# Kernel optimization log

Hardware: AMD Instinct MI355X
Metric: run time of the kernel (lower is better)

Reference implementation:

```python
import jax, jax.numpy as jnp
import numpy as np

EMB = 1024
HEADS = 16
EPS = 1e-6


def setup_inputs() -> dict:
    key = jax.random.key(0)
    ks = jax.random.split(key, 11)
    B, T = 4, 2048
    s = 0.02
    inp = {
        "x": jax.random.normal(ks[0], (B, T, EMB), dtype=jnp.float32),
        "Wq": jax.random.normal(ks[1], (EMB, EMB), dtype=jnp.float32) * s,
        "bq": jnp.zeros((EMB,), dtype=jnp.float32),
        "Wk": jax.random.normal(ks[2], (EMB, EMB), dtype=jnp.float32) * s,
        "bk": jnp.zeros((EMB,), dtype=jnp.float32),
        "Wv": jax.random.normal(ks[3], (EMB, EMB), dtype=jnp.float32) * s,
        "bv": jnp.zeros((EMB,), dtype=jnp.float32),
        "Wp": jax.random.normal(ks[4], (EMB, EMB), dtype=jnp.float32) * s,
        "bp": jnp.zeros((EMB,), dtype=jnp.float32),
        "gamma": jnp.ones((EMB,), dtype=jnp.float32),
        "beta": jnp.zeros((EMB,), dtype=jnp.float32),
    }
    return inp


def reference(x, Wq, bq, Wk, bk, Wv, bv, Wp, bp, gamma, beta):
    B, T, E = x.shape
    H = HEADS
    hd = E // H
    residual = x
    # torch Linear: y = x @ W.T + b
    q = (jnp.einsum('bte,fe->btf', x, Wq) + bq).reshape(B, T, H, hd).transpose(0, 2, 1, 3)
    k = (jnp.einsum('bte,fe->btf', x, Wk) + bk).reshape(B, T, H, hd).transpose(0, 2, 1, 3)
    v = (jnp.einsum('bte,fe->btf', x, Wv) + bv).reshape(B, T, H, hd).transpose(0, 2, 1, 3)
    # NOTE: original scales by 1/sqrt(T), not 1/sqrt(head_size)
    scale = 1.0 / jnp.sqrt(jnp.asarray(T, dtype=x.dtype))
    att = jnp.einsum('bhqd,bhkd->bhqk', q, k) * scale
    causal = jnp.tril(jnp.ones((T, T), dtype=bool))
    att = jnp.where(causal, att, -jnp.inf)
    att = jax.nn.softmax(att, axis=-1)
    out = jnp.einsum('bhqk,bhkd->bhqd', att, v)
    out = out.transpose(0, 2, 1, 3).reshape(B, T, E)
    # residual added BEFORE projection (as in original)
    out = jnp.einsum('bte,fe->btf', out + residual, Wp) + bp
    # LayerNorm(eps=1e-6)
    mu = jnp.mean(out, axis=-1, keepdims=True)
    var = jnp.mean(jnp.square(out - mu), axis=-1, keepdims=True)
    out = (out - mu) / jnp.sqrt(var + EPS) * gamma + beta
    return out
```

## Files before the change

### kernel.cpp

```cpp
#include <hip/hip_runtime.h>
#include <hip/hip_bf16.h>
#include <cstdint>
#include <cstdio>

#define EMB    1024
#define HEADS  16
#define HD     64
#define TSEQ   2048
#define NBATCH 4
#define BT     (NBATCH*TSEQ)
#define QKVN   3072
#define QKLD   2048

#define CSCALE (1.4426950408889634f * 0.022097086912079608f)

typedef __hip_bfloat16 bf16;
typedef __attribute__((ext_vector_type(8))) short short8;
typedef __attribute__((ext_vector_type(4))) short short4v;
typedef __attribute__((ext_vector_type(4))) float f32x4;

#define MFMA32(A,B,C) __builtin_amdgcn_mfma_f32_16x16x32_bf16(A,B,C,0,0,0)
#if __has_builtin(__builtin_amdgcn_mfma_f32_16x16x16_bf16)
#define MFMA16(A,B,C) __builtin_amdgcn_mfma_f32_16x16x16_bf16(A,B,C,0,0,0)
#else
#define MFMA16(A,B,C) __builtin_amdgcn_mfma_f32_16x16x16bf16_1k(A,B,C,0,0,0)
#endif

#if __has_builtin(__builtin_amdgcn_exp2f)
#define EXP2(x) __builtin_amdgcn_exp2f(x)
#else
#define EXP2(x) exp2f(x)
#endif

template<bool B> struct BoolC { static constexpr bool value = B; };

__device__ __forceinline__ void gload_lds16(const void* g, void* l) {
  __builtin_amdgcn_global_load_lds(
      (const __attribute__((address_space(1))) void*)g,
      (__attribute__((address_space(3))) void*)l,
      16, 0, 0);
}

__device__ __forceinline__ unsigned pkbf(float a, float b) {
  unsigned ua = __builtin_bit_cast(unsigned, a) + 0x8000u;
  unsigned ub = __builtin_bit_cast(unsigned, b) + 0x8000u;
  return __builtin_amdgcn_perm(ub, ua, 0x07060302u);
}

#define BARRIER() do { asm volatile("" ::: "memory"); \
                       __builtin_amdgcn_s_barrier(); \
                       asm volatile("" ::: "memory"); } while (0)
#define BAR_VM(N) do { asm volatile("s_waitcnt vmcnt(" #N ")" ::: "memory"); \
                       __builtin_amdgcn_s_barrier(); \
                       asm volatile("" ::: "memory"); } while (0)

__global__ void fused_cast(const float* __restrict__ x, const float* __restrict__ Wq,
                           const float* __restrict__ Wk, const float* __restrict__ Wv,
                           const float* __restrict__ Wp, const float* __restrict__ bq,
                           const float* __restrict__ bk, const float* __restrict__ bv,
                           bf16* __restrict__ xb, bf16* __restrict__ wqkv,
                           bf16* __restrict__ wpb, float* __restrict__ biasqkv) {
  const int blk = blockIdx.x;
  const int i = threadIdx.x * 4;
  if (blk >= 12288) {
    const int wsel = blk - 12288;
    const float* bsrc = wsel == 0 ? bq : (wsel == 1 ? bk : bv);
    float4 bv4 = *(const float4*)(bsrc + i);
    if (wsel == 0) { bv4.x *= CSCALE; bv4.y *= CSCALE; bv4.z *= CSCALE; bv4.w *= CSCALE; }
    *(float4*)(biasqkv + wsel * 1024 + i) = bv4;
    return;
  }
  const float* src; bf16* dst; float sc = 1.0f;
  if (blk < 8192)       { src = x  + (size_t)blk * 1024;           dst = xb   + (size_t)blk * 1024; }
  else if (blk < 9216)  { src = Wq + (size_t)(blk - 8192) * 1024;  dst = wqkv + (size_t)(blk - 8192) * 1024; sc = CSCALE; }
  else if (blk < 10240) { src = Wk + (size_t)(blk - 9216) * 1024;  dst = wqkv + ((size_t)1 << 20) + (size_t)(blk - 9216) * 1024; }
  else if (blk < 11264) { src = Wv + (size_t)(blk - 10240) * 1024; dst = wqkv + ((size_t)2 << 20) + (size_t)(blk - 10240) * 1024; }
  else                  { src = Wp + (size_t)(blk - 11264) * 1024; dst = wpb  + (size_t)(blk - 11264) * 1024; }
  float4 v = *(const float4*)(src + i);
  union { short4v v; bf16 b[4]; } u;
  u.b[0] = __float2bfloat16(v.x * sc); u.b[1] = __float2bfloat16(v.y * sc);
  u.b[2] = __float2bfloat16(v.z * sc); u.b[3] = __float2bfloat16(v.w * sc);
  *(short4v*)(dst + i) = u.v;
}

#define PHASE_MFMA(MI0, NJ0) do { \
  __builtin_amdgcn_s_setprio(1); \
  _Pragma("unroll") \
  for (int m2 = 0; m2 < 4; ++m2) { \
    _Pragma("unroll") \
    for (int n2 = 0; n2 < 2; ++n2) { \
      acc[(MI0)+m2][(NJ0)+n2] = MFMA32(af[m2][0], bfr[(NJ0)+n2][0], acc[(MI0)+m2][(NJ0)+n2]); \
      acc[(MI0)+m2][(NJ0)+n2] = MFMA32(af[m2][1], bfr[(NJ0)+n2][1], acc[(MI0)+m2][(NJ0)+n2]); \
    } \
  } \
  __builtin_amdgcn_s_setprio(0); \
} while (0)

#define TILE(T, P) { \
  const int kn = ((T) + 1) * 64; \
  const bool st = (T) < 15; \
  const char* aB = rdA + (P) * 32768; \
  const char* bB = rdB + (P) * 32768; \
  char* sA = ldsA + ((P) ^ 1) * 32768 + wbase; \
  char* sB = ldsB + ((P) ^ 1) * 32768 + wbase; \
   \
  _Pragma("unroll") \
  for (int m2 = 0; m2 < 4; ++m2) { \
    af[m2][0] = *(const short8*)(aB + m2 * 2048 + cs0); \
    af[m2][1] = *(const short8*)(aB + m2 * 2048 + cs1); \
  } \
  _Pragma("unroll") \
  for (int n2 = 0; n2 < 2; ++n2) { \
    bfr[n2][0] = *(const short8*)(bB + n2 * 2048 + cs0); \
    bfr[n2][1] = *(const short8*)(bB + n2 * 2048 + cs1); \
  } \
  if (st) { gload_lds16(gB + kn,          sB);         \
            gload_lds16(gB + 131072 + kn, sB + 16384); } \
  BARRIER(); \
  PHASE_MFMA(0, 0); \
  BARRIER(); \
   \
  _Pragma("unroll") \
  for (int n2 = 2; n2 < 4; ++n2) { \
    bfr[n2][0] = *(const short8*)(bB + n2 * 2048 + cs0); \
    bfr[n2][1] = *(const short8*)(bB + n2 * 2048 + cs1); \
  } \
  if (st) { gload_lds16(gA + kn,          sA);         \
            gload_lds16(gA + 131072 + kn, sA + 16384); } \
  BARRIER(); \
  PHASE_MFMA(0, 2); \
  if (st) { BAR_VM(4); } else { BAR_VM(0); } \
   \
  _Pragma("unroll") \
  for (int m2 = 0; m2 < 4; ++m2) { \
    af[m2][0] = *(const short8*)(aB + (4 + m2) * 2048 + cs0); \
    af[m2][1] = *(const short8*)(aB + (4 + m2) * 2048 + cs1); \
  } \
  if (st) { gload_lds16(gB + 65536 + kn,  sB + 8192);  \
            gload_lds16(gB + 196608 + kn, sB + 24576); } \
  BARRIER(); \
  PHASE_MFMA(4, 2); \
  BARRIER(); \
   \
  if (st) { gload_lds16(gA + 65536 + kn,  sA + 8192);  \
            gload_lds16(gA + 196608 + kn, sA + 24576); } \
  PHASE_MFMA(4, 0); \
  if (st) { BAR_VM(2); } \
}

__global__ __launch_bounds__(512, 2) void gemm_qkv8(
    const bf16* __restrict__ A, const bf16* __restrict__ B,
    const float* __restrict__ bias, bf16* __restrict__ qkout,
    bf16* __restrict__ vt) {
  __shared__ short smem[65536];
  const int tid = threadIdx.x;
  const int l = tid & 63, w = tid >> 6;
  const int r = l & 15, qd = l >> 4;
  const int wm = w >> 2, wn = w & 3;

  const int f0 = blockIdx.x;
  const int sid = (f0 & 7) * 48 + (f0 >> 3);
  const int m0 = (sid / 12) * 256;
  const int n0 = (sid % 12) * 256;

  const int rowA = tid >> 3;
  const int chk = (tid & 7) ^ (rowA & 7);
  const bf16* gA = A + (size_t)(m0 + rowA) * 1024 + chk * 8;
  const bf16* gB = B + (size_t)(n0 + rowA) * 1024 + chk * 8;
  char* ldsA = (char*)smem;
  char* ldsB = (char*)smem + 65536;
  const int wbase = w * 1024;

  const char* rdA = (const char*)smem + wm * 16384 + r * 128;
  const char* rdB = (const char*)smem + 65536 + (wn >> 1) * 16384 +
                    ((wn & 1) * 64 + r) * 128;
  const int cs0 = (qd ^ (r & 7)) * 16;
  const int cs1 = ((4 + qd) ^ (r & 7)) * 16;

  f32x4 acc[8][4];
#pragma unroll
  for (int i = 0; i < 8; ++i)
#pragma unroll
    for (int j = 0; j < 4; ++j) acc[i][j] = (f32x4){0.f, 0.f, 0.f, 0.f};
  short8 af[4][2], bfr[4][2];

  {
    char* sA = ldsA + wbase;
    char* sB = ldsB + wbase;
    gload_lds16(gB,          sB);
    gload_lds16(gB + 131072, sB + 16384);
    gload_lds16(gA,          sA);
    gload_lds16(gA + 131072, sA + 16384);
    gload_lds16(gB + 65536,  sB + 8192);
    gload_lds16(gB + 196608, sB + 24576);
    gload_lds16(gA + 65536,  sA + 8192);
    gload_lds16(gA + 196608, sA + 24576);
    BAR_VM(2);
  }

#pragma unroll 1
  for (int tt = 0; tt < 8; ++tt) {
    TILE(tt * 2, 0)
    TILE(tt * 2 + 1, 1)
  }

  if (n0 < 2048) {
#pragma unroll
    for (int nt = 0; nt < 4; ++nt) {
      const int col = n0 + wn * 64 + nt * 16 + r;
      const float bv = bias[col];
#pragma unroll
      for (int mi = 0; mi < 8; ++mi) {
#pragma unroll
        for (int reg = 0; reg < 4; ++reg) {
          const int row = m0 + wm * 128 + mi * 16 + qd * 4 + reg;
          qkout[(size_t)row * QKLD + col] = __float2bfloat16(acc[mi][nt][reg] + bv);
        }
      }
    }
  } else {
    char* img = (char*)smem;
#pragma unroll
    for (int nt = 0; nt < 4; ++nt) {
      const int c_local = wn * 64 + nt * 16 + r;
      const float bv = bias[n0 + c_local];
      const int d7 = c_local & 7;
#pragma unroll
      for (int mi = 0; mi < 8; ++mi) {
        const int tbase = wm * 128 + mi * 16 + qd * 4;
        const int chunk = tbase >> 6;
        const int sbits = ((tbase >> 3) ^ d7) & 7;
        union { short4v v; bf16 b[4]; } u;
#pragma unroll
        for (int reg = 0; reg < 4; ++reg)
          u.b[reg] = __float2bfloat16(acc[mi][nt][reg] + bv);
        *(short4v*)(img + c_local * 512 + chunk * 128 + sbits * 16 + (qd & 1) * 8) = u.v;
      }
    }
    __syncthreads();
    const int bb = m0 >> 11, tb = m0 & 2047;
    const int hb = (n0 - 2048) >> 6;
    const int off = (tid & 31) * 16;
#pragma unroll
    for (int i = 0; i < 16; ++i) {
      const int row = i * 16 + (tid >> 5);
      const int h2 = hb + (row >> 6), d = row & 63;
      const f32x4 vv = *(const f32x4*)(img + row * 512 + off);
      char* dst = (char*)(vt + ((size_t)(bb * 16 + h2) * 64 + d) * 2048 + tb) + off;
      *(f32x4*)dst = vv;
    }
  }
}

#define PJ_MFMA(MI0) do { \
  __builtin_amdgcn_s_setprio(1); \
  _Pragma("unroll") \
  for (int m2 = 0; m2 < 2; ++m2) { \
    _Pragma("unroll") \
    for (int nj = 0; nj < 2; ++nj) { \
      acc[(MI0)+m2][nj] = MFMA32(af[m2][0], bfr[nj][0], acc[(MI0)+m2][nj]); \
      acc[(MI0)+m2][nj] = MFMA32(af[m2][1], bfr[nj][1], acc[(MI0)+m2][nj]); \
    } \
  } \
  __builtin_amdgcn_s_setprio(0); \
} while (0)

#define PJ_TILE(T, P) { \
  const int kn = ((T) + 1) * 64; \
  const bool st = (T) < 15; \
  const char* aB = rdA + (P) * 32768; \
  const char* bB = rdB + (P) * 16384; \
  char* sA = ldsA + ((P) ^ 1) * 32768 + wbase; \
  char* sB = ldsB + ((P) ^ 1) * 16384 + wbase; \
   \
  _Pragma("unroll") \
  for (int m2 = 0; m2 < 2; ++m2) { \
    af[m2][0] = *(const short8*)(aB + m2 * 2048 + cs0); \
    af[m2][1] = *(const short8*)(aB + m2 * 2048 + cs1); \
  } \
  _Pragma("unroll") \
  for (int nj = 0; nj < 2; ++nj) { \
    bfr[nj][0] = *(const short8*)(bB + nj * 2048 + cs0); \
    bfr[nj][1] = *(const short8*)(bB + nj * 2048 + cs1); \
  } \
  if (st) { gload_lds16(gB + kn,         sB); \
            gload_lds16(gB + 65536 + kn, sB + 8192); } \
  BARRIER(); \
  PJ_MFMA(0); \
  BARRIER(); \
   \
  _Pragma("unroll") \
  for (int m2 = 0; m2 < 2; ++m2) { \
    af[m2][0] = *(const short8*)(aB + (2 + m2) * 2048 + cs0); \
    af[m2][1] = *(const short8*)(aB + (2 + m2) * 2048 + cs1); \
  } \
  if (st) { gload_lds16(gA + kn,          sA); \
            gload_lds16(gA + 131072 + kn, sA + 16384); } \
  BARRIER(); \
  PJ_MFMA(2); \
  if (st) { BAR_VM(4); } else { BAR_VM(0); } \
   \
  _Pragma("unroll") \
  for (int m2 = 0; m2 < 2; ++m2) { \
    af[m2][0] = *(const short8*)(aB + (4 + m2) * 2048 + cs0); \
    af[m2][1] = *(const short8*)(aB + (4 + m2) * 2048 + cs1); \
  } \
  if (st) { gload_lds16(gA + 65536 + kn,  sA + 8192); \
            gload_lds16(gA + 196608 + kn, sA + 24576); } \
  BARRIER(); \
  PJ_MFMA(4); \
  BARRIER(); \
   \
  _Pragma("unroll") \
  for (int m2 = 0; m2 < 2; ++m2) { \
    af[m2][0] = *(const short8*)(aB + (6 + m2) * 2048 + cs0); \
    af[m2][1] = *(const short8*)(aB + (6 + m2) * 2048 + cs1); \
  } \
  PJ_MFMA(6); \
  if (st) { BAR_VM(2); } \
}

__global__ __launch_bounds__(512, 2) void gemm_proj8(
    const bf16* __restrict__ A, const bf16* __restrict__ B,
    const float* __restrict__ bias, float* __restrict__ out) {
  __shared__ short smem[49152];
  const int tid = threadIdx.x;
  const int l = tid & 63, w = tid >> 6;
  const int r = l & 15, qd = l >> 4;
  const int wm = w >> 2, wn = w & 3;

  const int f0 = blockIdx.x;
  const int sid = (f0 & 7) * 32 + (f0 >> 3);
  const int m0 = (sid >> 3) * 256;
  const int n0 = (sid & 7) * 128;

  const int rowA = tid >> 3;
  const int chk = (tid & 7) ^ (rowA & 7);
  const bf16* gA = A + (size_t)(m0 + rowA) * 1024 + chk * 8;
  const bf16* gB = B + (size_t)(n0 + rowA) * 1024 + chk * 8;
  char* ldsA = (char*)smem;
  char* ldsB = (char*)smem + 65536;
  const int wbase = w * 1024;

  const char* rdA = (const char*)smem + wm * 16384 + r * 128;
  const char* rdB = (const char*)smem + 65536 + (wn * 32 + r) * 128;
  const int cs0 = (qd ^ (r & 7)) * 16;
  const int cs1 = ((4 + qd) ^ (r & 7)) * 16;

  f32x4 acc[8][2];
#pragma unroll
  for (int i = 0; i < 8; ++i)
#pragma unroll
    for (int j = 0; j < 2; ++j) acc[i][j] = (f32x4){0.f, 0.f, 0.f, 0.f};
  short8 af[2][2], bfr[2][2];

  {
    char* sA = ldsA + wbase;
    char* sB = ldsB + wbase;
    gload_lds16(gB,          sB);
    gload_lds16(gB + 65536,  sB + 8192);
    gload_lds16(gA,          sA);
    gload_lds16(gA + 131072, sA + 16384);
    gload_lds16(gA + 65536,  sA + 8192);
    gload_lds16(gA + 196608, sA + 24576);
    BAR_VM(2);
  }

#pragma unroll 1
  for (int tt = 0; tt < 8; ++tt) {
    PJ_TILE(tt * 2, 0)
    PJ_TILE(tt * 2 + 1, 1)
  }

#pragma unroll
  for (int nj = 0; nj < 2; ++nj) {
    const int col = n0 + wn * 32 + nj * 16 + r;
    const float bv = bias[col];
#pragma unroll
    for (int mi = 0; mi < 8; ++mi) {
#pragma unroll
      for (int reg = 0; reg < 4; ++reg) {
        const int row = m0 + wm * 128 + mi * 16 + qd * 4 + reg;
        out[(size_t)row * 1024 + col] = acc[mi][nj][reg] + bv;
      }
    }
  }
}

__global__ __launch_bounds__(256, 2) void flash7(
    const bf16* __restrict__ qk, const bf16* __restrict__ vt,
    const float* __restrict__ x, bf16* __restrict__ pb) {
  const int bh = blockIdx.x;
  const int ip = blockIdx.y;
  const int b = bh >> 4, h = bh & 15;
  const int qt[4] = { 31 - ip, 23 - ip, ip + 8, ip };
  const int tid = threadIdx.x, l = tid & 63, w = tid >> 6;
  const int r = l & 15, quad = l >> 4;

  __shared__ bf16 VtL[2][64 * 64];

  const bf16* Qbase = qk + (size_t)b * TSEQ * QKLD + h * HD;
  const bf16* Kbase = Qbase + 1024;
  const bf16* Vhead = vt + (size_t)bh * 64 * 2048;

  const int sl0 = tid, sl1 = 256 + tid;
  const bf16* vg0 = Vhead + (size_t)(sl0 >> 3) * 2048 + (sl0 & 7) * 8;
  const bf16* vg1 = Vhead + (size_t)(sl1 >> 3) * 2048 + (sl1 & 7) * 8;
  char* ldsb0[2] = { (char*)&VtL[0][0] + w * 1024, (char*)&VtL[1][0] + w * 1024 };
  char* ldsb1[2] = { (char*)&VtL[0][0] + 4096 + w * 1024, (char*)&VtL[1][0] + 4096 + w * 1024 };

  short8 qf0[4], qf1[4];
#pragma unroll
  for (int t = 0; t < 4; ++t) {
    const bf16* qp = Qbase + (size_t)(qt[t] * 64 + w * 16 + r) * QKLD + quad * 8;
    qf0[t] = *(const short8*)qp;
    qf1[t] = *(const short8*)(qp + 32);
  }

  f32x4 o[4][4], lac[4];
#pragma unroll
  for (int t = 0; t < 4; ++t) {
    lac[t] = (f32x4){0.f, 0.f, 0.f, 0.f};
#pragma unroll
    for (int nt = 0; nt < 4; ++nt) o[t][nt] = (f32x4){0.f, 0.f, 0.f, 0.f};
  }

  short4v ones4;
#pragma unroll
  for (int j = 0; j < 4; ++j) ones4[j] = (short)0x3F80;

  short4v vf[4][4];

  const bf16* Kl = Kbase + (size_t)r * QKLD + quad * 8;
  auto loadK = [&](int kt, short8 (&k0)[4], short8 (&k1)[4]) {
#pragma unroll
    for (int g = 0; g < 4; ++g) {
      const bf16* kp = Kl + (size_t)(kt * 64 + g * 16) * QKLD;
      k0[g] = *(const short8*)kp;
      k1[g] = *(const short8*)(kp + 32);
    }
  };

  short8 kA0[4], kA1[4], kB0[4], kB1[4];

  gload_lds16(vg0, ldsb0[0]);
  gload_lds16(vg1, ldsb1[0]);
  loadK(0, kA0, kA1);
  int bsel = 0;

  const int ktmax = qt[0];
  const int qrow_l = w * 16 + r;

  auto tilestep = [&](int t, auto diagc, short8 (&k0)[4], short8 (&k1)[4],
                      int kt) {
    constexpr bool D = decltype(diagc)::value;
    f32x4 s[4];
    __builtin_amdgcn_s_setprio(1);
#pragma unroll
    for (int g = 0; g < 4; ++g) {
      f32x4 a = (f32x4){0.f, 0.f, 0.f, 0.f};
      a = MFMA32(k0[g], qf0[t], a);
      a = MFMA32(k1[g], qf1[t], a);
      s[g] = a;
    }
    __builtin_amdgcn_s_setprio(0);
    short4v pA[4];
#pragma unroll
    for (int g = 0; g < 4; ++g) {
      float p[4];
#pragma unroll
      for (int reg = 0; reg < 4; ++reg) {
        float e = EXP2(s[g][reg]);
        if (D) {
          const int kj = g * 16 + quad * 4 + reg;
          if (kj > qrow_l) e = 0.f;
        }
        p[reg] = e;
      }
      union { short4v v; unsigned u[2]; } pu;
      pu.u[0] = pkbf(p[0], p[1]);
      pu.u[1] = pkbf(p[2], p[3]);
      pA[g] = pu.v;
    }
    __builtin_amdgcn_s_setprio(1);
#pragma unroll
    for (int nt = 0; nt < 4; ++nt)
#pragma unroll
      for (int g = 0; g < 4; ++g)
        o[t][nt] = MFMA16(pA[g], vf[nt][g], o[t][nt]);
#pragma unroll
    for (int g = 0; g < 4; ++g)
      lac[t] = MFMA16(pA[g], ones4, lac[t]);
    __builtin_amdgcn_s_setprio(0);
  };

  auto ktbody = [&](int kt, short8 (&kc0)[4], short8 (&kc1)[4],
                    short8 (&kn0)[4], short8 (&kn1)[4]) {
    __syncthreads();
    if (kt < ktmax) {
      gload_lds16(vg0 + (kt + 1) * 64, ldsb0[bsel ^ 1]);
      gload_lds16(vg1 + (kt + 1) * 64, ldsb1[bsel ^ 1]);
      loadK(kt + 1, kn0, kn1);
    }
    {
      const bf16* V = &VtL[bsel][0];
#pragma unroll
      for (int nt = 0; nt < 4; ++nt)
#pragma unroll
        for (int g = 0; g < 4; ++g)
          vf[nt][g] = *(const short4v*)(V + (nt * 16 + r) * 64 +
                                        (((g * 2 + (quad >> 1)) ^ (r & 7)) * 8) + (quad & 1) * 4);
    }
    if (kt == qt[0]) tilestep(0, BoolC<true>{}, kc0, kc1, kt);
    else             tilestep(0, BoolC<false>{}, kc0, kc1, kt);
    if (kt <= qt[1]) { if (kt == qt[1]) tilestep(1, BoolC<true>{}, kc0, kc1, kt);
                       else             tilestep(1, BoolC<false>{}, kc0, kc1, kt); }
    if (kt <= qt[2]) { if (kt == qt[2]) tilestep(2, BoolC<true>{}, kc0, kc1, kt);
                       else             tilestep(2, BoolC<false>{}, kc0, kc1, kt); }
    if (kt <= qt[3]) { if (kt == qt[3]) tilestep(3, BoolC<true>{}, kc0, kc1, kt);
                       else             tilestep(3, BoolC<false>{}, kc0, kc1, kt); }
    bsel ^= 1;
  };

  int kt = 0;
#pragma unroll 1
  for (; kt + 1 <= ktmax; kt += 2) {
    ktbody(kt,     kA0, kA1, kB0, kB1);
    ktbody(kt + 1, kB0, kB1, kA0, kA1);
  }
  if (kt <= ktmax) ktbody(kt, kA0, kA1, kB0, kB1);

#pragma unroll
  for (int t = 0; t < 4; ++t) {
#pragma unroll
    for (int reg = 0; reg < 4; ++reg) {
      const float inv = 1.0f / lac[t][reg];
      const int row = qt[t] * 64 + w * 16 + quad * 4 + reg;
      const float* xr = x + (size_t)(b * TSEQ + row) * EMB + h * HD;
      bf16* pr = pb + (size_t)(b * TSEQ + row) * EMB + h * HD;
#pragma unroll
      for (int nt = 0; nt < 4; ++nt) {
        const int d = nt * 16 + r;
        pr[d] = __float2bfloat16(o[t][nt][reg] * inv + xr[d]);
      }
    }
  }
}

__global__ __launch_bounds__(256) void ln_kernel(float* __restrict__ out,
                                                 const float* __restrict__ gamma,
                                                 const float* __restrict__ beta) {
  const int row = blockIdx.x;
  const int tid = threadIdx.x;
  float* p = out + (size_t)row * EMB;
  float4 v = ((const float4*)p)[tid];
  float s = v.x + v.y + v.z + v.w;
  float ss = v.x * v.x + v.y * v.y + v.z * v.z + v.w * v.w;
#pragma unroll
  for (int m = 1; m < 64; m <<= 1) {
    s += __shfl_xor(s, m, 64);
    ss += __shfl_xor(ss, m, 64);
  }
  __shared__ float red[8];
  const int w = tid >> 6, l = tid & 63;
  if (l == 0) { red[w] = s; red[4 + w] = ss; }
  __syncthreads();
  s = red[0] + red[1] + red[2] + red[3];
  ss = red[4] + red[5] + red[6] + red[7];
  const float mu = s * (1.0f / EMB);
  const float var = ss * (1.0f / EMB) - mu * mu;
  const float rs = rsqrtf(var + 1e-6f);
  const float4 g = ((const float4*)gamma)[tid];
  const float4 bb = ((const float4*)beta)[tid];
  float4 o;
  o.x = (v.x - mu) * rs * g.x + bb.x;
  o.y = (v.y - mu) * rs * g.y + bb.y;
  o.z = (v.z - mu) * rs * g.z + bb.z;
  o.w = (v.w - mu) * rs * g.w + bb.w;
  ((float4*)p)[tid] = o;
}

extern "C" void kernel_launch(void* const* d_in, const int* in_sizes, int n_in,
                              void* d_out, int out_size, void* d_ws, size_t ws_size,
                              hipStream_t stream) {
  const float* x     = (const float*)d_in[0];
  const float* Wq    = (const float*)d_in[1];
  const float* bq    = (const float*)d_in[2];
  const float* Wk    = (const float*)d_in[3];
  const float* bk    = (const float*)d_in[4];
  const float* Wv    = (const float*)d_in[5];
  const float* bv    = (const float*)d_in[6];
  const float* Wp    = (const float*)d_in[7];
  const float* bp    = (const float*)d_in[8];
  const float* gamma = (const float*)d_in[9];
  const float* beta  = (const float*)d_in[10];
  float* out = (float*)d_out;

  if (ws_size < (size_t)74 * 1024 * 1024) {
    printf("kernel_launch: ws_size %zu too small\n", ws_size);
    return;
  }
  char* ws = (char*)d_ws;
  bf16* xb    = (bf16*)ws;
  bf16* wqkv  = (bf16*)(ws + ((size_t)16 << 20));
  bf16* wpb   = (bf16*)(ws + ((size_t)22 << 20));
  float* bqkv = (float*)(ws + ((size_t)24 << 20));
  bf16* qkbuf = (bf16*)(ws + ((size_t)25 << 20));
  bf16* vtbuf = (bf16*)(ws + ((size_t)57 << 20));
  bf16* pbuf  = xb;

  fused_cast<<<12291, 256, 0, stream>>>(x, Wq, Wk, Wv, Wp, bq, bk, bv, xb, wqkv, wpb, bqkv);

  gemm_qkv8<<<dim3(384), dim3(512), 0, stream>>>(xb, wqkv, bqkv, qkbuf, vtbuf);

  flash7<<<dim3(64, 8), 256, 0, stream>>>(qkbuf, vtbuf, x, pbuf);

  gemm_proj8<<<dim3(256), dim3(512), 0, stream>>>(pbuf, wpb, bp, out);

  ln_kernel<<<BT, 256, 0, stream>>>(out, gamma, beta);
}
```

Before: 275.0 us.

## Split key tiles across two wave groups in flash kernel with LDS combine

The flash attention kernel now runs 512 threads per block, and two groups of four waves process alternating key tiles (even and odd) for the same query tiles. Each group accumulates partial O and row sums, which are merged through shared memory before normalization and the residual store. V staging becomes a four-slot LDS ring loaded two tiles ahead, and the K register double-buffering is dropped in favor of direct per-iteration loads. The aim is more parallelism per (batch, head) and better latency hiding. The cost is extra barriers, a larger LDS footprint, an LDS reduction pass, and possible idle waves on odd tile counts.

```diff
diff --git a/kernel.cpp b/kernel.cpp
--- a/kernel.cpp
+++ b/kernel.cpp
@@ -387,7 +387,7 @@
   }
 }
 
-__global__ __launch_bounds__(256, 2) void flash7(
+__global__ __launch_bounds__(512, 2) void flash8(
     const bf16* __restrict__ qk, const bf16* __restrict__ vt,
     const float* __restrict__ x, bf16* __restrict__ pb) {
   const int bh = blockIdx.x;
@@ -395,24 +395,22 @@
   const int b = bh >> 4, h = bh & 15;
   const int qt[4] = { 31 - ip, 23 - ip, ip + 8, ip };
   const int tid = threadIdx.x, l = tid & 63, w = tid >> 6;
+  const int wg = w & 3, grp = w >> 2;
   const int r = l & 15, quad = l >> 4;
 
-  __shared__ bf16 VtL[2][64 * 64];
+  __shared__ __align__(16) char smem[40960];
 
   const bf16* Qbase = qk + (size_t)b * TSEQ * QKLD + h * HD;
   const bf16* Kbase = Qbase + 1024;
   const bf16* Vhead = vt + (size_t)bh * 64 * 2048;
 
-  const int sl0 = tid, sl1 = 256 + tid;
-  const bf16* vg0 = Vhead + (size_t)(sl0 >> 3) * 2048 + (sl0 & 7) * 8;
-  const bf16* vg1 = Vhead + (size_t)(sl1 >> 3) * 2048 + (sl1 & 7) * 8;
-  char* ldsb0[2] = { (char*)&VtL[0][0] + w * 1024, (char*)&VtL[1][0] + w * 1024 };
-  char* ldsb1[2] = { (char*)&VtL[0][0] + 4096 + w * 1024, (char*)&VtL[1][0] + 4096 + w * 1024 };
+  const bf16* vg = Vhead + (size_t)(tid >> 3) * 2048 + (tid & 7) * 8;
+  char* vdst = smem + w * 1024;
 
   short8 qf0[4], qf1[4];
 #pragma unroll
   for (int t = 0; t < 4; ++t) {
-    const bf16* qp = Qbase + (size_t)(qt[t] * 64 + w * 16 + r) * QKLD + quad * 8;
+    const bf16* qp = Qbase + (size_t)(qt[t] * 64 + wg * 16 + r) * QKLD + quad * 8;
     qf0[t] = *(const short8*)qp;
     qf1[t] = *(const short8*)(qp + 32);
   }
@@ -432,27 +430,13 @@
   short4v vf[4][4];
 
   const bf16* Kl = Kbase + (size_t)r * QKLD + quad * 8;
-  auto loadK = [&](int kt, short8 (&k0)[4], short8 (&k1)[4]) {
-#pragma unroll
-    for (int g = 0; g < 4; ++g) {
-      const bf16* kp = Kl + (size_t)(kt * 64 + g * 16) * QKLD;
-      k0[g] = *(const short8*)kp;
-      k1[g] = *(const short8*)(kp + 32);
-    }
-  };
-
-  short8 kA0[4], kA1[4], kB0[4], kB1[4];
-
-  gload_lds16(vg0, ldsb0[0]);
-  gload_lds16(vg1, ldsb1[0]);
-  loadK(0, kA0, kA1);
-  int bsel = 0;
-
   const int ktmax = qt[0];
-  const int qrow_l = w * 16 + r;
-
-  auto tilestep = [&](int t, auto diagc, short8 (&k0)[4], short8 (&k1)[4],
-                      int kt) {
+  const int qrow_l = wg * 16 + r;
+
+  gload_lds16(vg, vdst);
+  gload_lds16(vg + 64, vdst + 8192);
+
+  auto tilestep = [&](int t, auto diagc, short8 (&k0)[4], short8 (&k1)[4]) {
     constexpr bool D = decltype(diagc)::value;
     f32x4 s[4];
     __builtin_amdgcn_s_setprio(1);
@@ -494,56 +478,92 @@
     __builtin_amdgcn_s_setprio(0);
   };
 
-  auto ktbody = [&](int kt, short8 (&kc0)[4], short8 (&kc1)[4],
-                    short8 (&kn0)[4], short8 (&kn1)[4]) {
+  const int niter = (ktmax >> 1) + 1;
+#pragma unroll 1
+  for (int i = 0; i < niter; ++i) {
+    const int kt = 2 * i + grp;
+    const bool act = kt <= ktmax;
+    short8 k0[4], k1[4];
+    if (act) {
+#pragma unroll
+      for (int g = 0; g < 4; ++g) {
+        const bf16* kp = Kl + (size_t)(kt * 64 + g * 16) * QKLD;
+        k0[g] = *(const short8*)kp;
+        k1[g] = *(const short8*)(kp + 32);
+      }
+    }
     __syncthreads();
-    if (kt < ktmax) {
-      gload_lds16(vg0 + (kt + 1) * 64, ldsb0[bsel ^ 1]);
-      gload_lds16(vg1 + (kt + 1) * 64, ldsb1[bsel ^ 1]);
-      loadK(kt + 1, kn0, kn1);
-    }
-    {
-      const bf16* V = &VtL[bsel][0];
+    if (2 * i + 2 <= ktmax)
+      gload_lds16(vg + (2 * i + 2) * 64, smem + ((2 * i + 2) & 3) * 8192 + w * 1024);
+    if (2 * i + 3 <= ktmax)
+      gload_lds16(vg + (2 * i + 3) * 64, smem + ((2 * i + 3) & 3) * 8192 + w * 1024);
+    if (act) {
+      const bf16* V = (const bf16*)smem + (kt & 3) * 4096;
 #pragma unroll
       for (int nt = 0; nt < 4; ++nt)
 #pragma unroll
         for (int g = 0; g < 4; ++g)
           vf[nt][g] = *(const short4v*)(V + (nt * 16 + r) * 64 +
                                         (((g * 2 + (quad >> 1)) ^ (r & 7)) * 8) + (quad & 1) * 4);
-    }
-    if (kt == qt[0]) tilestep(0, BoolC<true>{}, kc0, kc1, kt);
-    else             tilestep(0, BoolC<false>{}, kc0, kc1, kt);
-    if (kt <= qt[1]) { if (kt == qt[1]) tilestep(1, BoolC<true>{}, kc0, kc1, kt);
-                       else             tilestep(1, BoolC<false>{}, kc0, kc1, kt); }
-    if (kt <= qt[2]) { if (kt == qt[2]) tilestep(2, BoolC<true>{}, kc0, kc1, kt);
-                       else             tilestep(2, BoolC<false>{}, kc0, kc1, kt); }
-    if (kt <= qt[3]) { if (kt == qt[3]) tilestep(3, BoolC<true>{}, kc0, kc1, kt);
-                       else             tilestep(3, BoolC<false>{}, kc0, kc1, kt); }
-    bsel ^= 1;
-  };
-
-  int kt = 0;
-#pragma unroll 1
-  for (; kt + 1 <= ktmax; kt += 2) {
-    ktbody(kt,     kA0, kA1, kB0, kB1);
-    ktbody(kt + 1, kB0, kB1, kA0, kA1);
-  }
-  if (kt <= ktmax) ktbody(kt, kA0, kA1, kB0, kB1);
-
-#pragma unroll
-  for (int t = 0; t < 4; ++t) {
-#pragma unroll
-    for (int reg = 0; reg < 4; ++reg) {
-      const float inv = 1.0f / lac[t][reg];
-      const int row = qt[t] * 64 + w * 16 + quad * 4 + reg;
-      const float* xr = x + (size_t)(b * TSEQ + row) * EMB + h * HD;
-      bf16* pr = pb + (size_t)(b * TSEQ + row) * EMB + h * HD;
-#pragma unroll
-      for (int nt = 0; nt < 4; ++nt) {
-        const int d = nt * 16 + r;
-        pr[d] = __float2bfloat16(o[t][nt][reg] * inv + xr[d]);
+      if (kt == qt[0]) tilestep(0, BoolC<true>{}, k0, k1);
+      else             tilestep(0, BoolC<false>{}, k0, k1);
+      if (kt <= qt[1]) { if (kt == qt[1]) tilestep(1, BoolC<true>{}, k0, k1);
+                         else             tilestep(1, BoolC<false>{}, k0, k1); }
+      if (kt <= qt[2]) { if (kt == qt[2]) tilestep(2, BoolC<true>{}, k0, k1);
+                         else             tilestep(2, BoolC<false>{}, k0, k1); }
+      if (kt <= qt[3]) { if (kt == qt[3]) tilestep(3, BoolC<true>{}, k0, k1);
+                         else             tilestep(3, BoolC<false>{}, k0, k1); }
+    }
+  }
+
+  float* combO = (float*)smem;
+  float* combL = (float*)(smem + 32768);
+  const int lb128 = (wg * 64 + l) * 32;
+  const int lbl = (wg * 64 + l) * 8;
+
+  __syncthreads();
+#pragma unroll
+  for (int rnd = 0; rnd < 2; ++rnd) {
+    const int wgrp = (rnd == 0) ? 1 : 0;
+    if (grp == wgrp) {
+#pragma unroll
+      for (int t2 = 0; t2 < 2; ++t2) {
+        const int tt = rnd * 2 + t2;
+#pragma unroll
+        for (int nt = 0; nt < 4; ++nt)
+          *(f32x4*)&combO[lb128 + (((t2 * 4 + nt) ^ (l & 7)) << 2)] = o[tt][nt];
+        *(f32x4*)&combL[lbl + t2 * 4] = lac[tt];
       }
     }
+    __syncthreads();
+    if (grp != wgrp) {
+#pragma unroll
+      for (int t2 = 0; t2 < 2; ++t2) {
+        const int tt = rnd * 2 + t2;
+        const f32x4 ls = *(const f32x4*)&combL[lbl + t2 * 4];
+#pragma unroll
+        for (int j2 = 0; j2 < 4; ++j2) lac[tt][j2] += ls[j2];
+#pragma unroll
+        for (int nt = 0; nt < 4; ++nt) {
+          const f32x4 ov = *(const f32x4*)&combO[lb128 + (((t2 * 4 + nt) ^ (l & 7)) << 2)];
+#pragma unroll
+          for (int j2 = 0; j2 < 4; ++j2) o[tt][nt][j2] += ov[j2];
+        }
+#pragma unroll
+        for (int reg = 0; reg < 4; ++reg) {
+          const float inv = 1.0f / lac[tt][reg];
+          const int row = qt[tt] * 64 + wg * 16 + quad * 4 + reg;
+          const float* xr = x + (size_t)(b * TSEQ + row) * EMB + h * HD;
+          bf16* pr = pb + (size_t)(b * TSEQ + row) * EMB + h * HD;
+#pragma unroll
+          for (int nt = 0; nt < 4; ++nt) {
+            const int d = nt * 16 + r;
+            pr[d] = __float2bfloat16(o[tt][nt][reg] * inv + xr[d]);
+          }
+        }
+      }
+    }
+    if (rnd == 0) __syncthreads();
   }
 }
 
@@ -613,7 +633,7 @@
 
   gemm_qkv8<<<dim3(384), dim3(512), 0, stream>>>(xb, wqkv, bqkv, qkbuf, vtbuf);
 
-  flash7<<<dim3(64, 8), 256, 0, stream>>>(qkbuf, vtbuf, x, pbuf);
+  flash8<<<dim3(64, 8), 512, 0, stream>>>(qkbuf, vtbuf, x, pbuf);
 
   gemm_proj8<<<dim3(256), dim3(512), 0, stream>>>(pbuf, wpb, bp, out);
 
```

Measured after the change: 304.0 us. 10.5% more time.
